# Optimization experiments

Hardware: AMD Instinct MI355X
Metric: run time of the kernel (lower is better)

Reference implementation:

```python
import jax, jax.numpy as jnp
import numpy as np

N = 16384      # total nodes
B = 8          # graphs in batch
NPG = N // B   # nodes per graph
E = 262144     # edges
IN, HID, OUT = 128, 256, 128
ICP_ITERS = 10


def setup_inputs():
    key = jax.random.key(0)
    ks = jax.random.split(key, 12)
    x = jax.random.normal(ks[0], (N, IN), jnp.float32)
    # random edges kept within each graph (offsets per graph)
    src = jax.random.randint(ks[1], (E,), 0, NPG, dtype=jnp.int32)
    dst = jax.random.randint(ks[2], (E,), 0, NPG, dtype=jnp.int32)
    goff = (jnp.arange(E, dtype=jnp.int32) % B) * NPG
    edge_index = jnp.stack([src + goff, dst + goff], 0)
    pos = jax.random.normal(ks[3], (N, 3), jnp.float32)
    batch = jnp.repeat(jnp.arange(B, dtype=jnp.int32), NPG)
    def lin(k, fi, fo):
        return jax.random.normal(k, (fi, fo), jnp.float32) * (fi ** -0.5)
    return dict(
        x=x, edge_index=edge_index, pos=pos, batch=batch,
        W1=lin(ks[4], IN, HID),  b1=jnp.zeros((HID,), jnp.float32),
        W2=lin(ks[5], HID, HID), b2=jnp.zeros((HID,), jnp.float32),
        W3=lin(ks[6], HID, OUT), b3=jnp.zeros((OUT,), jnp.float32),
        Wt=lin(ks[7], OUT, 3),   bt=jnp.zeros((3,), jnp.float32),
    )


def gcn_conv(x, W, b, row, col, n):
    # GCNConv: symmetric norm with self loops; messages flow row->col
    xw = x @ W
    loop = jnp.arange(n, dtype=row.dtype)
    r = jnp.concatenate([row, loop])
    c = jnp.concatenate([col, loop])
    deg = jax.ops.segment_sum(jnp.ones_like(c, dtype=xw.dtype), c, num_segments=n)
    dinv = jnp.where(deg > 0, jax.lax.rsqrt(jnp.maximum(deg, 1e-12)), 0.0)
    norm = dinv[r] * dinv[c]
    out = jax.ops.segment_sum(xw[r] * norm[:, None], c, num_segments=n)
    return out + b


def pdist2(a, b):
    # squared pairwise distances [n,m]
    return (jnp.sum(a * a, -1)[:, None] + jnp.sum(b * b, -1)[None, :]
            - 2.0 * (a @ b.T))


def icp_align(src, tgt):
    # fixed-iteration batched ICP (Kabsch/SVD per iteration)
    for _ in range(ICP_ITERS):
        d = pdist2(jax.lax.stop_gradient(src), jax.lax.stop_gradient(tgt))
        idx = jnp.argmin(d, axis=1)
        corr = tgt[idx]
        cs = jnp.mean(src, 0)
        cc = jnp.mean(corr, 0)
        H = (src - cs).T @ (corr - cc)  # [3,3]
        U, S, Vt = jnp.linalg.svd(H, full_matrices=False)
        sign = jnp.sign(jnp.linalg.det(Vt.T @ U.T))
        D = jnp.stack([jnp.ones_like(sign), jnp.ones_like(sign), sign])
        R = (Vt.T * D[None, :]) @ U.T
        t = cc - R @ cs
        src = src @ R.T + t
    return src


def chamfer(a, b):
    d = pdist2(jax.lax.stop_gradient(a), jax.lax.stop_gradient(b))
    ia = jnp.argmin(d, 1)
    ib = jnp.argmin(d, 0)
    d1 = jnp.mean(jnp.sum((a - b[ia]) ** 2, -1))
    d2 = jnp.mean(jnp.sum((b - a[ib]) ** 2, -1))
    return d1 + d2


def reference(x, edge_index, pos, batch, W1, b1, W2, b2, W3, b3, Wt, bt):
    n = x.shape[0]
    row, col = edge_index[0], edge_index[1]
    h = jax.nn.relu(gcn_conv(x, W1, b1, row, col, n))
    h = jax.nn.relu(gcn_conv(h, W2, b2, row, col, n))
    h = gcn_conv(h, W3, b3, row, col, n)
    pos_offset = h @ Wt + bt
    tpos = pos + pos_offset
    nb = int(batch[-1]) + 1          # sorted, equal-size graphs
    npg = n // nb
    src = tpos.reshape(nb, npg, 3)
    tgt = pos.reshape(nb, npg, 3)
    aligned = jax.vmap(icp_align)(src, tgt)
    loss = jnp.mean(jax.vmap(chamfer)(aligned, tgt))
    return h, aligned.reshape(n, 3), loss
```

## Files before the change

kernel.cpp:

```cpp
#include <hip/hip_runtime.h>
#include <math.h>

#define N_NODES 16384
#define B_GRAPHS 8
#define NPG_     2048
#define E_EDGES  262144
#define F_IN  128
#define F_HID 256
#define F_OUT 128
#define ICP_IT 10

typedef __attribute__((ext_vector_type(8))) short bf16x8;
typedef __attribute__((ext_vector_type(4))) float f32x4;

__device__ __forceinline__ float b2f(unsigned short u) {
    union { unsigned int u; float f; } v; v.u = ((unsigned int)u) << 16; return v.f;
}
__device__ __forceinline__ unsigned short f2b(float f) {
    union { float f; unsigned int u; } v; v.f = f;
    unsigned int r = v.u + 0x7FFFu + ((v.u >> 16) & 1u);
    return (unsigned short)(r >> 16);
}
__device__ __forceinline__ int swz32(int i) {
    return (i & ~31) | ((i & 31) ^ ((i >> 5) & 31));
}
__device__ __forceinline__ void st_agent(float* p, float v) {
    __hip_atomic_store(p, v, __ATOMIC_RELAXED, __HIP_MEMORY_SCOPE_AGENT);
}
__device__ __forceinline__ float ld_agent(const float* p) {
    return __hip_atomic_load(p, __ATOMIC_RELAXED, __HIP_MEMORY_SCOPE_AGENT);
}
__device__ __forceinline__ void st_agent_i(int* p, int v) {
    __hip_atomic_store(p, v, __ATOMIC_RELAXED, __HIP_MEMORY_SCOPE_AGENT);
}
__device__ __forceinline__ int ld_agent_i(const int* p) {
    return __hip_atomic_load(p, __ATOMIC_RELAXED, __HIP_MEMORY_SCOPE_AGENT);
}

__global__ __launch_bounds__(256) void k_prep(
    const float* __restrict__ x, unsigned short* __restrict__ xb,
    const float* __restrict__ W1, const float* __restrict__ W2, const float* __restrict__ W3,
    unsigned short* __restrict__ W1b, unsigned short* __restrict__ W2b, unsigned short* __restrict__ W3b,
    const int* __restrict__ col, int* __restrict__ counts)
{
    const int b = blockIdx.x, tid = threadIdx.x;
    if (b < 2048) {
        int i = b * 256 + tid;
        float4 v = ((const float4*)x)[i];
        uint2 o;
        o.x = (unsigned int)f2b(v.x) | ((unsigned int)f2b(v.y) << 16);
        o.y = (unsigned int)f2b(v.z) | ((unsigned int)f2b(v.w) << 16);
        ((uint2*)xb)[i] = o;
    } else if (b < 2176) {
        int idx = (b - 2048) * 256 + tid;
        int k = idx >> 8, n = idx & 255;
        W1b[n * 128 + k] = f2b(W1[idx]);
    } else if (b < 2432) {
        int idx = (b - 2176) * 256 + tid;
        int k = idx >> 8, n = idx & 255;
        W2b[n * 256 + k] = f2b(W2[idx]);
    } else if (b < 2560) {
        int idx = (b - 2432) * 256 + tid;
        int k = idx >> 7, n = idx & 127;
        W3b[n * 256 + k] = f2b(W3[idx]);
    } else {
        int e = (b - 2560) * 256 + tid;
        atomicAdd(&counts[col[e]], 1);
    }
}

__global__ __launch_bounds__(1024) void k_scan(const int* __restrict__ counts,
        int* __restrict__ offs, int* __restrict__ cursor, float* __restrict__ dinv)
{
    __shared__ int wtot[16];
    const int t = threadIdx.x;
    const int base = t * 16;
    int local[16];
    int s = 0;
#pragma unroll
    for (int i = 0; i < 16; i++) { local[i] = counts[base + i]; s += local[i]; }
    const int lane = t & 63, w = t >> 6;
    int inc = s;
    for (int o = 1; o < 64; o <<= 1) {
        int v = __shfl_up(inc, o);
        if (lane >= o) inc += v;
    }
    if (lane == 63) wtot[w] = inc;
    __syncthreads();
    if (t < 16) {
        int v = wtot[t];
        for (int o = 1; o < 16; o <<= 1) {
            int u = __shfl_up(v, o);
            if (t >= o) v += u;
        }
        wtot[t] = v;
    }
    __syncthreads();
    int run = (w > 0 ? wtot[w - 1] : 0) + (inc - s);
#pragma unroll
    for (int i = 0; i < 16; i++) {
        offs[base + i]   = run;
        cursor[base + i] = run;
        dinv[base + i]   = rsqrtf((float)(local[i] + 1));
        run += local[i];
    }
    if (t == 1023) offs[N_NODES] = run;
}

__global__ void k_scatter(const int* __restrict__ row, const int* __restrict__ col,
        int* __restrict__ cursor, const float* __restrict__ dinv,
        int* __restrict__ srcid, float* __restrict__ normv)
{
    int e = blockIdx.x * 256 + threadIdx.x;
    if (e >= E_EDGES) return;
    int r = row[e], c = col[e];
    int p = atomicAdd(&cursor[c], 1);
    srcid[p] = r;
    normv[p] = dinv[r] * dinv[c];
}

template<int OUTF, int FUSET>
__global__ __launch_bounds__(128) void k_agg128(const unsigned short* __restrict__ X,
        void* __restrict__ Y,
        const int* __restrict__ offs, const int* __restrict__ srcid,
        const float* __restrict__ normv, const float* __restrict__ dinv,
        const float* __restrict__ bias, int relu,
        const float* __restrict__ Wt, const float* __restrict__ bt,
        const float* __restrict__ pos, float* __restrict__ tposO)
{
    const int local = threadIdx.x >> 6;
    const int n = blockIdx.x * 2 + local;
    const int j = threadIdx.x & 63;
    const unsigned int* Xu = (const unsigned int*)X;
    float di = dinv[n];
    float w0 = di * di;
    unsigned int v = Xu[(size_t)n * 64 + j];
    float a0 = b2f((unsigned short)v) * w0;
    float a1 = b2f((unsigned short)(v >> 16)) * w0;
    int p = offs[n];
    const int p1 = offs[n + 1];
    for (; p + 3 < p1; p += 4) {
        int s0i = srcid[p], s1i = srcid[p + 1], s2i = srcid[p + 2], s3i = srcid[p + 3];
        float n0 = normv[p], n1 = normv[p + 1], n2 = normv[p + 2], n3 = normv[p + 3];
        unsigned int v0 = Xu[(size_t)s0i * 64 + j];
        unsigned int v1 = Xu[(size_t)s1i * 64 + j];
        unsigned int v2 = Xu[(size_t)s2i * 64 + j];
        unsigned int v3 = Xu[(size_t)s3i * 64 + j];
        a0 = fmaf(b2f((unsigned short)v0), n0, a0);
        a1 = fmaf(b2f((unsigned short)(v0 >> 16)), n0, a1);
        a0 = fmaf(b2f((unsigned short)v1), n1, a0);
        a1 = fmaf(b2f((unsigned short)(v1 >> 16)), n1, a1);
        a0 = fmaf(b2f((unsigned short)v2), n2, a0);
        a1 = fmaf(b2f((unsigned short)(v2 >> 16)), n2, a1);
        a0 = fmaf(b2f((unsigned short)v3), n3, a0);
        a1 = fmaf(b2f((unsigned short)(v3 >> 16)), n3, a1);
    }
    for (; p < p1; ++p) {
        unsigned int va = Xu[(size_t)srcid[p] * 64 + j]; float na = normv[p];
        a0 = fmaf(b2f((unsigned short)va), na, a0);
        a1 = fmaf(b2f((unsigned short)(va >> 16)), na, a1);
    }
    if (bias) { a0 += bias[2 * j]; a1 += bias[2 * j + 1]; }
    if (relu) { a0 = fmaxf(a0, 0.f); a1 = fmaxf(a1, 0.f); }
    if (OUTF) {
        float* Yf = (float*)Y;
        Yf[(size_t)n * 128 + 2 * j]     = a0;
        Yf[(size_t)n * 128 + 2 * j + 1] = a1;
    } else {
        ((unsigned int*)Y)[(size_t)n * 64 + j] =
            (unsigned int)f2b(a0) | ((unsigned int)f2b(a1) << 16);
    }
    if (FUSET) {
        float wt0 = Wt[6 * j + 0], wt1 = Wt[6 * j + 1], wt2 = Wt[6 * j + 2];
        float wt3 = Wt[6 * j + 3], wt4 = Wt[6 * j + 4], wt5 = Wt[6 * j + 5];
        float s0 = a0 * wt0 + a1 * wt3;
        float s1 = a0 * wt1 + a1 * wt4;
        float s2 = a0 * wt2 + a1 * wt5;
        for (int o = 32; o > 0; o >>= 1) {
            s0 += __shfl_down(s0, o);
            s1 += __shfl_down(s1, o);
            s2 += __shfl_down(s2, o);
        }
        if (j == 0) {
            tposO[n * 3 + 0] = pos[n * 3 + 0] + s0 + bt[0];
            tposO[n * 3 + 1] = pos[n * 3 + 1] + s1 + bt[1];
            tposO[n * 3 + 2] = pos[n * 3 + 2] + s2 + bt[2];
        }
    }
}

__global__ __launch_bounds__(128) void k_agg256(const unsigned short* __restrict__ X,
        unsigned short* __restrict__ Y,
        const int* __restrict__ offs, const int* __restrict__ srcid,
        const float* __restrict__ normv, const float* __restrict__ dinv,
        const float* __restrict__ bias, int relu)
{
    const int local = threadIdx.x >> 6;
    const int n = blockIdx.x * 2 + local;
    const int lane = threadIdx.x & 63;
    const uint2* Xu = (const uint2*)X;
    float di = dinv[n];
    float w0 = di * di;
    uint2 v = Xu[(size_t)n * 64 + lane];
    float a0 = b2f((unsigned short)v.x) * w0;
    float a1 = b2f((unsigned short)(v.x >> 16)) * w0;
    float a2 = b2f((unsigned short)v.y) * w0;
    float a3 = b2f((unsigned short)(v.y >> 16)) * w0;
    int p = offs[n];
    const int p1 = offs[n + 1];
    for (; p + 3 < p1; p += 4) {
        int s0i = srcid[p], s1i = srcid[p + 1], s2i = srcid[p + 2], s3i = srcid[p + 3];
        float n0 = normv[p], n1 = normv[p + 1], n2 = normv[p + 2], n3 = normv[p + 3];
        uint2 v0 = Xu[(size_t)s0i * 64 + lane];
        uint2 v1 = Xu[(size_t)s1i * 64 + lane];
        uint2 v2 = Xu[(size_t)s2i * 64 + lane];
        uint2 v3 = Xu[(size_t)s3i * 64 + lane];
        a0 = fmaf(b2f((unsigned short)v0.x), n0, a0);
        a1 = fmaf(b2f((unsigned short)(v0.x >> 16)), n0, a1);
        a2 = fmaf(b2f((unsigned short)v0.y), n0, a2);
        a3 = fmaf(b2f((unsigned short)(v0.y >> 16)), n0, a3);
        a0 = fmaf(b2f((unsigned short)v1.x), n1, a0);
        a1 = fmaf(b2f((unsigned short)(v1.x >> 16)), n1, a1);
        a2 = fmaf(b2f((unsigned short)v1.y), n1, a2);
        a3 = fmaf(b2f((unsigned short)(v1.y >> 16)), n1, a3);
        a0 = fmaf(b2f((unsigned short)v2.x), n2, a0);
        a1 = fmaf(b2f((unsigned short)(v2.x >> 16)), n2, a1);
        a2 = fmaf(b2f((unsigned short)v2.y), n2, a2);
        a3 = fmaf(b2f((unsigned short)(v2.y >> 16)), n2, a3);
        a0 = fmaf(b2f((unsigned short)v3.x), n3, a0);
        a1 = fmaf(b2f((unsigned short)(v3.x >> 16)), n3, a1);
        a2 = fmaf(b2f((unsigned short)v3.y), n3, a2);
        a3 = fmaf(b2f((unsigned short)(v3.y >> 16)), n3, a3);
    }
    for (; p < p1; ++p) {
        uint2 va = Xu[(size_t)srcid[p] * 64 + lane]; float na = normv[p];
        a0 = fmaf(b2f((unsigned short)va.x), na, a0);
        a1 = fmaf(b2f((unsigned short)(va.x >> 16)), na, a1);
        a2 = fmaf(b2f((unsigned short)va.y), na, a2);
        a3 = fmaf(b2f((unsigned short)(va.y >> 16)), na, a3);
    }
    if (bias) {
        float4 bv = ((const float4*)bias)[lane];
        a0 += bv.x; a1 += bv.y; a2 += bv.z; a3 += bv.w;
    }
    if (relu) {
        a0 = fmaxf(a0, 0.f); a1 = fmaxf(a1, 0.f);
        a2 = fmaxf(a2, 0.f); a3 = fmaxf(a3, 0.f);
    }
    uint2 o;
    o.x = (unsigned int)f2b(a0) | ((unsigned int)f2b(a1) << 16);
    o.y = (unsigned int)f2b(a2) | ((unsigned int)f2b(a3) << 16);
    ((uint2*)Y)[(size_t)n * 64 + lane] = o;
}

__global__ __launch_bounds__(256) void k_gemm_bf16(
    const unsigned short* __restrict__ A,
    const unsigned short* __restrict__ Bt,
    const float* __restrict__ bias, unsigned short* __restrict__ C,
    int M, int N, int K, int relu)
{
    __shared__ __align__(16) unsigned short As[128 * 64];
    __shared__ __align__(16) unsigned short Bs[64 * 64];
    const int tid  = threadIdx.x;
    const int lane = tid & 63;
    const int wave = tid >> 6;
    const int bm = blockIdx.y * 128, bn = blockIdx.x * 64;
    const int wm = (wave >> 1) * 64, wn = (wave & 1) * 32;
    f32x4 acc[4][2];
#pragma unroll
    for (int mf = 0; mf < 4; mf++)
#pragma unroll
        for (int nf = 0; nf < 2; nf++) acc[mf][nf] = (f32x4){0.f, 0.f, 0.f, 0.f};

    for (int k0 = 0; k0 < K; k0 += 64) {
#pragma unroll
        for (int i = 0; i < 4; i++) {
            int idx = i * 256 + tid;
            int m = idx >> 3, slot = idx & 7;
            const unsigned short* src = A + (size_t)(bm + m) * K + k0 + ((slot ^ (m & 7)) << 3);
            __builtin_amdgcn_global_load_lds(
                (const __attribute__((address_space(1))) unsigned int*)src,
                (__attribute__((address_space(3))) unsigned int*)(As + (size_t)i * 2048 + wave * 512),
                16, 0, 0);
        }
#pragma unroll
        for (int i = 0; i < 2; i++) {
            int idx = i * 256 + tid;
            int n = idx >> 3, slot = idx & 7;
            const unsigned short* src = Bt + (size_t)(bn + n) * K + k0 + ((slot ^ (n & 7)) << 3);
            __builtin_amdgcn_global_load_lds(
                (const __attribute__((address_space(1))) unsigned int*)src,
                (__attribute__((address_space(3))) unsigned int*)(Bs + (size_t)i * 2048 + wave * 512),
                16, 0, 0);
        }
        __syncthreads();
        bf16x8 af[4][2], bfr[2][2];
        const int qd = lane >> 4;
#pragma unroll
        for (int s = 0; s < 2; s++) {
#pragma unroll
            for (int mf = 0; mf < 4; mf++) {
                int m = wm + mf * 16 + (lane & 15);
                int slot = (s * 4 + qd) ^ (m & 7);
                af[mf][s] = *(const bf16x8*)(As + m * 64 + slot * 8);
            }
#pragma unroll
            for (int nf = 0; nf < 2; nf++) {
                int n = wn + nf * 16 + (lane & 15);
                int slot = (s * 4 + qd) ^ (n & 7);
                bfr[nf][s] = *(const bf16x8*)(Bs + n * 64 + slot * 8);
            }
        }
#pragma unroll
        for (int s = 0; s < 2; s++)
#pragma unroll
            for (int mf = 0; mf < 4; mf++)
#pragma unroll
                for (int nf = 0; nf < 2; nf++)
                    acc[mf][nf] = __builtin_amdgcn_mfma_f32_16x16x32_bf16(
                        af[mf][s], bfr[nf][s], acc[mf][nf], 0, 0, 0);
        __syncthreads();
    }
#pragma unroll
    for (int nf = 0; nf < 2; nf++) {
        int col = bn + wn + nf * 16 + (lane & 15);
        float bv = bias ? bias[col] : 0.f;
#pragma unroll
        for (int mf = 0; mf < 4; mf++) {
#pragma unroll
            for (int r = 0; r < 4; r++) {
                int row = bm + wm + mf * 16 + (lane >> 4) * 4 + r;
                float v = acc[mf][nf][r] + bv;
                if (relu) v = fmaxf(v, 0.f);
                C[(size_t)row * N + col] = f2b(v);
            }
        }
    }
}

__global__ __launch_bounds__(512) void k_icp_all(
    const float* __restrict__ tpos, const float* __restrict__ pos,
    float* __restrict__ partials,
    float* __restrict__ chpart,
    int* __restrict__ ctrs,
    float* __restrict__ out_aligned, float* __restrict__ out_loss)
{
    const int g = blockIdx.x & 7, blk = blockIdx.x >> 3;
    const int myline = g * 32 + blk;
    const int tid = threadIdx.x;
    const int wave = tid >> 6, lane = tid & 63;
    __shared__ float4 tq[NPG_];
    __shared__ __align__(16) unsigned char scratch[NPG_ * 16];
    float* sm_d = (float*)scratch;
    unsigned short* sm_i = (unsigned short*)(scratch + 64 * 65 * 4);
    float4* al = (float4*)scratch;
    __shared__ float ssx[64], ssy[64], ssz[64];
    __shared__ float wred[8][2];
    __shared__ float Tsh[12];
    __shared__ int lastFlag;

    for (int i = tid; i < NPG_; i += 512) {
        const float* p = &pos[(size_t)(g * NPG_ + i) * 3];
        float qx = p[0], qy = p[1], qz = p[2];
        tq[swz32(i)] = make_float4(qx, qy, qz, fmaf(qx, qx, fmaf(qy, qy, qz * qz)));
    }
    if (tid < 12) Tsh[tid] = (tid == 0 || tid == 4 || tid == 8) ? 1.f : 0.f;
    float Px[8], Py[8], Pz[8];
#pragma unroll
    for (int u = 0; u < 8; u++) {
        int n = g * NPG_ + blk * 64 + wave * 8 + u;
        Px[u] = tpos[n * 3 + 0]; Py[u] = tpos[n * 3 + 1]; Pz[u] = tpos[n * 3 + 2];
    }
    double Td[12];
    if (tid == 0) {
#pragma unroll
        for (int k = 0; k < 12; k++) Td[k] = (k == 0 || k == 4 || k == 8) ? 1.0 : 0.0;
    }
    __syncthreads();

    for (int iter = 0; iter < ICP_IT; ++iter) {
        const int bufbase = (iter & 1) * 256;
        float Tf[12];
#pragma unroll
        for (int k = 0; k < 12; k++) Tf[k] = Tsh[k];
        float Sx[8], Sy[8], Sz[8], Tx[8], Ty[8], Tz[8], bd[8];
        int bi[8];
#pragma unroll
        for (int u = 0; u < 8; u++) {
            float X = Tf[0] * Px[u] + Tf[1] * Py[u] + Tf[2] * Pz[u] + Tf[9];
            float Y = Tf[3] * Px[u] + Tf[4] * Py[u] + Tf[5] * Pz[u] + Tf[10];
            float Z = Tf[6] * Px[u] + Tf[7] * Py[u] + Tf[8] * Pz[u] + Tf[11];
            Sx[u] = X; Sy[u] = Y; Sz[u] = Z;
            Tx[u] = -2.f * X; Ty[u] = -2.f * Y; Tz[u] = -2.f * Z;
            bd[u] = 1e30f; bi[u] = lane * 32;
        }
        const int qbase = lane * 32;
        for (int j = 0; j < 32; j++) {
            float4 t4 = tq[qbase + (j ^ (lane & 31))];
            int idx = qbase + j;
#pragma unroll
            for (int u = 0; u < 8; u++) {
                float d = fmaf(Tx[u], t4.x, fmaf(Ty[u], t4.y, fmaf(Tz[u], t4.z, t4.w)));
                if (d < bd[u]) { bd[u] = d; bi[u] = idx; }
            }
        }
#pragma unroll
        for (int u = 0; u < 8; u++) {
            int row = wave * 8 + u;
            sm_d[row * 65 + lane] = bd[u];
            sm_i[row * 65 + lane] = (unsigned short)bi[u];
            if (lane == u) { ssx[row] = Sx[u]; ssy[row] = Sy[u]; ssz[row] = Sz[u]; }
        }
        __syncthreads();
        if (wave == 0) {
            const int s = tid;
            float best = sm_d[s * 65];
            int ib = sm_i[s * 65];
            for (int r = 1; r < 64; r++) {
                float dd = sm_d[s * 65 + r];
                int ii = sm_i[s * 65 + r];
                if (dd < best) { best = dd; ib = ii; }
            }
            float4 c = tq[swz32(ib)];
            float X = ssx[s], Y = ssy[s], Z = ssz[s];
            float vals[15] = { X, Y, Z, c.x, c.y, c.z,
                               X * c.x, X * c.y, X * c.z,
                               Y * c.x, Y * c.y, Y * c.z,
                               Z * c.x, Z * c.y, Z * c.z };
#pragma unroll
            for (int k = 0; k < 15; k++) {
                float v = vals[k];
                for (int o = 32; o > 0; o >>= 1) v += __shfl_down(v, o);
                if (lane == 0) st_agent(&partials[((size_t)bufbase + myline) * 16 + k], v);
            }
            if (lane == 0) {
                asm volatile("s_waitcnt vmcnt(0)" ::: "memory");
                st_agent_i((int*)partials + ((size_t)bufbase + myline) * 16 + 15, iter + 1);
            }
            double sd[15];
#pragma unroll
            for (int k = 0; k < 15; k++) sd[k] = 0.0;
            if (lane < 32) {
                const float* lp = partials + ((size_t)bufbase + g * 32 + lane) * 16;
                while (ld_agent_i((const int*)lp + 15) < iter + 1) __builtin_amdgcn_s_sleep(1);
                asm volatile("" ::: "memory");
#pragma unroll
                for (int k = 0; k < 15; k++) sd[k] = (double)ld_agent(lp + k);
            }
#pragma unroll
            for (int k = 0; k < 15; k++) {
                for (int o = 16; o > 0; o >>= 1) sd[k] += __shfl_down(sd[k], o);
            }
            if (lane == 0) {
                const double n = (double)NPG_;
                const double rin = 1.0 / (double)NPG_;
                double cs0 = sd[0] * rin, cs1 = sd[1] * rin, cs2 = sd[2] * rin;
                double cc0 = sd[3] * rin, cc1 = sd[4] * rin, cc2 = sd[5] * rin;
                float H[3][3];
                H[0][0] = (float)(sd[6]  - n * cs0 * cc0); H[0][1] = (float)(sd[7]  - n * cs0 * cc1); H[0][2] = (float)(sd[8]  - n * cs0 * cc2);
                H[1][0] = (float)(sd[9]  - n * cs1 * cc0); H[1][1] = (float)(sd[10] - n * cs1 * cc1); H[1][2] = (float)(sd[11] - n * cs1 * cc2);
                H[2][0] = (float)(sd[12] - n * cs2 * cc0); H[2][1] = (float)(sd[13] - n * cs2 * cc1); H[2][2] = (float)(sd[14] - n * cs2 * cc2);
                double R[3][3];
                float fn = 1e-30f;
                for (int i = 0; i < 3; i++) for (int j2 = 0; j2 < 3; j2++) fn += H[i][j2] * H[i][j2];
                float sc = rsqrtf(fn);
                float Xm[3][3];
                for (int i = 0; i < 3; i++) for (int j2 = 0; j2 < 3; j2++) Xm[i][j2] = H[i][j2] * sc;
                float dX = Xm[0][0] * (Xm[1][1]*Xm[2][2] - Xm[1][2]*Xm[2][1])
                         - Xm[0][1] * (Xm[1][0]*Xm[2][2] - Xm[1][2]*Xm[2][0])
                         + Xm[0][2] * (Xm[1][0]*Xm[2][1] - Xm[1][1]*Xm[2][0]);
                if (dX > 1e-4f) {
                    for (int itn = 0; itn < 16; ++itn) {
                        float C00 = Xm[1][1]*Xm[2][2] - Xm[1][2]*Xm[2][1];
                        float C01 = Xm[1][2]*Xm[2][0] - Xm[1][0]*Xm[2][2];
                        float C02 = Xm[1][0]*Xm[2][1] - Xm[1][1]*Xm[2][0];
                        float C10 = Xm[2][1]*Xm[0][2] - Xm[2][2]*Xm[0][1];
                        float C11 = Xm[2][2]*Xm[0][0] - Xm[2][0]*Xm[0][2];
                        float C12 = Xm[2][0]*Xm[0][1] - Xm[2][1]*Xm[0][0];
                        float C20 = Xm[0][1]*Xm[1][2] - Xm[0][2]*Xm[1][1];
                        float C21 = Xm[0][2]*Xm[1][0] - Xm[0][0]*Xm[1][2];
                        float C22 = Xm[0][0]*Xm[1][1] - Xm[0][1]*Xm[1][0];
                        float det = Xm[0][0]*C00 + Xm[0][1]*C01 + Xm[0][2]*C02;
                        if (fabsf(det) < 1e-30f) break;
                        float rd = 0.5f / det;
                        Xm[0][0] = 0.5f*Xm[0][0] + C00*rd; Xm[0][1] = 0.5f*Xm[0][1] + C01*rd; Xm[0][2] = 0.5f*Xm[0][2] + C02*rd;
                        Xm[1][0] = 0.5f*Xm[1][0] + C10*rd; Xm[1][1] = 0.5f*Xm[1][1] + C11*rd; Xm[1][2] = 0.5f*Xm[1][2] + C12*rd;
                        Xm[2][0] = 0.5f*Xm[2][0] + C20*rd; Xm[2][1] = 0.5f*Xm[2][1] + C21*rd; Xm[2][2] = 0.5f*Xm[2][2] + C22*rd;
                    }
                    for (int i = 0; i < 3; i++) for (int j2 = 0; j2 < 3; j2++) R[i][j2] = (double)Xm[j2][i];
                } else {
                    float A[3][3], V[3][3] = {{1,0,0},{0,1,0},{0,0,1}};
                    for (int i = 0; i < 3; i++)
                        for (int j2 = 0; j2 < 3; j2++)
                            A[i][j2] = H[0][i] * H[0][j2] + H[1][i] * H[1][j2] + H[2][i] * H[2][j2];
                    for (int sweep = 0; sweep < 8; ++sweep) {
                        for (int p = 0; p < 2; p++) for (int q = p + 1; q < 3; q++) {
                            float apq = A[p][q];
                            if (fabsf(apq) < 1e-30f) continue;
                            float theta = (A[q][q] - A[p][p]) / (2.f * apq);
                            float t = copysignf(1.f, theta) / (fabsf(theta) + sqrtf(theta * theta + 1.f));
                            float c2 = 1.f / sqrtf(t * t + 1.f);
                            float s2 = t * c2;
                            for (int k = 0; k < 3; k++) { float akp = A[k][p], akq = A[k][q]; A[k][p] = c2*akp - s2*akq; A[k][q] = s2*akp + c2*akq; }
                            for (int k = 0; k < 3; k++) { float apk = A[p][k], aqk = A[q][k]; A[p][k] = c2*apk - s2*aqk; A[q][k] = s2*apk + c2*aqk; }
                            for (int k = 0; k < 3; k++) { float vkp = V[k][p], vkq = V[k][q]; V[k][p] = c2*vkp - s2*vkq; V[k][q] = s2*vkp + c2*vkq; }
                        }
                    }
                    float lam[3] = { A[0][0], A[1][1], A[2][2] };
                    int ord[3] = { 0, 1, 2 };
                    if (lam[ord[1]] > lam[ord[0]]) { int t0 = ord[0]; ord[0] = ord[1]; ord[1] = t0; }
                    if (lam[ord[2]] > lam[ord[0]]) { int t0 = ord[0]; ord[0] = ord[2]; ord[2] = t0; }
                    if (lam[ord[2]] > lam[ord[1]]) { int t0 = ord[1]; ord[1] = ord[2]; ord[2] = t0; }
                    float vc[3][3], uc[3][3];
                    for (int i = 0; i < 3; i++) { vc[i][0] = V[0][ord[i]]; vc[i][1] = V[1][ord[i]]; vc[i][2] = V[2][ord[i]]; }
                    for (int i = 0; i < 3; i++) {
                        float u0 = H[0][0]*vc[i][0] + H[0][1]*vc[i][1] + H[0][2]*vc[i][2];
                        float u1 = H[1][0]*vc[i][0] + H[1][1]*vc[i][1] + H[1][2]*vc[i][2];
                        float u2 = H[2][0]*vc[i][0] + H[2][1]*vc[i][1] + H[2][2]*vc[i][2];
                        for (int j2 = 0; j2 < i; j2++) {
                            float dp = u0*uc[j2][0] + u1*uc[j2][1] + u2*uc[j2][2];
                            u0 -= dp*uc[j2][0]; u1 -= dp*uc[j2][1]; u2 -= dp*uc[j2][2];
                        }
                        float nn2 = sqrtf(u0*u0 + u1*u1 + u2*u2);
                        if (nn2 > 1e-12f) { uc[i][0] = u0/nn2; uc[i][1] = u1/nn2; uc[i][2] = u2/nn2; }
                        else if (i == 2) {
                            uc[2][0] = uc[0][1]*uc[1][2] - uc[0][2]*uc[1][1];
                            uc[2][1] = uc[0][2]*uc[1][0] - uc[0][0]*uc[1][2];
                            uc[2][2] = uc[0][0]*uc[1][1] - uc[0][1]*uc[1][0];
                        } else if (i == 1) {
                            float a0 = (fabsf(uc[0][0]) < 0.9f) ? 1.f : 0.f, a1 = 1.f - a0, a2 = 0.f;
                            float dp = a0*uc[0][0] + a1*uc[0][1] + a2*uc[0][2];
                            a0 -= dp*uc[0][0]; a1 -= dp*uc[0][1]; a2 -= dp*uc[0][2];
                            float nn3 = sqrtf(a0*a0 + a1*a1 + a2*a2);
                            uc[1][0] = a0/nn3; uc[1][1] = a1/nn3; uc[1][2] = a2/nn3;
                        } else { uc[0][0] = 1; uc[0][1] = 0; uc[0][2] = 0; }
                    }
                    float detU = uc[0][0]*(uc[1][1]*uc[2][2] - uc[1][2]*uc[2][1])
                               - uc[0][1]*(uc[1][0]*uc[2][2] - uc[1][2]*uc[2][0])
                               + uc[0][2]*(uc[1][0]*uc[2][1] - uc[1][1]*uc[2][0]);
                    float detV = vc[0][0]*(vc[1][1]*vc[2][2] - vc[1][2]*vc[2][1])
                               - vc[0][1]*(vc[1][0]*vc[2][2] - vc[1][2]*vc[2][0])
                               + vc[0][2]*(vc[1][0]*vc[2][1] - vc[1][1]*vc[2][0]);
                    float sgn = (detU * detV < 0.f) ? -1.f : 1.f;
                    for (int i = 0; i < 3; i++)
                        for (int j2 = 0; j2 < 3; j2++)
                            R[i][j2] = (double)(vc[0][i]*uc[0][j2] + vc[1][i]*uc[1][j2] + sgn * vc[2][i]*uc[2][j2]);
                }
                double tr0 = cc0 - (R[0][0]*cs0 + R[0][1]*cs1 + R[0][2]*cs2);
                double tr1 = cc1 - (R[1][0]*cs0 + R[1][1]*cs1 + R[1][2]*cs2);
                double tr2 = cc2 - (R[2][0]*cs0 + R[2][1]*cs1 + R[2][2]*cs2);
                double An[12];
                for (int i = 0; i < 3; i++)
                    for (int j2 = 0; j2 < 3; j2++)
                        An[i*3+j2] = R[i][0]*Td[0*3+j2] + R[i][1]*Td[1*3+j2] + R[i][2]*Td[2*3+j2];
                An[9]  = R[0][0]*Td[9] + R[0][1]*Td[10] + R[0][2]*Td[11] + tr0;
                An[10] = R[1][0]*Td[9] + R[1][1]*Td[10] + R[1][2]*Td[11] + tr1;
                An[11] = R[2][0]*Td[9] + R[2][1]*Td[10] + R[2][2]*Td[11] + tr2;
#pragma unroll
                for (int k = 0; k < 12; k++) { Td[k] = An[k]; Tsh[k] = (float)An[k]; }
            }
        }
        __syncthreads();
    }

    {
        float Tf[12];
#pragma unroll
        for (int k = 0; k < 12; k++) Tf[k] = Tsh[k];
        __syncthreads();
        for (int i = tid; i < NPG_; i += 512) {
            const float* q = &tpos[(size_t)(g * NPG_ + i) * 3];
            float X = Tf[0] * q[0] + Tf[1] * q[1] + Tf[2] * q[2] + Tf[9];
            float Y = Tf[3] * q[0] + Tf[4] * q[1] + Tf[5] * q[2] + Tf[10];
            float Z = Tf[6] * q[0] + Tf[7] * q[1] + Tf[8] * q[2] + Tf[11];
            al[swz32(i)] = make_float4(X, Y, Z, fmaf(X, X, fmaf(Y, Y, Z * Z)));
            if (blk == 0) {
                out_aligned[(size_t)(g * NPG_ + i) * 3 + 0] = X;
                out_aligned[(size_t)(g * NPG_ + i) * 3 + 1] = Y;
                out_aligned[(size_t)(g * NPG_ + i) * 3 + 2] = Z;
            }
        }
        __syncthreads();
        float Ax[8], Ay[8], Az[8], Aw[8], Qx[8], Qy[8], Qz[8], Qw[8], d1[8], d2[8];
#pragma unroll
        for (int u = 0; u < 8; u++) {
            int s = swz32(blk * 64 + wave * 8 + u);
            float4 a4 = al[s]; float4 p4 = tq[s];
            Ax[u] = -2.f * a4.x; Ay[u] = -2.f * a4.y; Az[u] = -2.f * a4.z; Aw[u] = a4.w;
            Qx[u] = -2.f * p4.x; Qy[u] = -2.f * p4.y; Qz[u] = -2.f * p4.z; Qw[u] = p4.w;
            d1[u] = 1e30f; d2[u] = 1e30f;
        }
        const int qbase = lane * 32;
        for (int j = 0; j < 32; j++) {
            int s = qbase + (j ^ (lane & 31));
            float4 t4 = tq[s];
            float4 b4 = al[s];
#pragma unroll
            for (int u = 0; u < 8; u++) {
                d1[u] = fminf(d1[u], fmaf(Ax[u], t4.x, fmaf(Ay[u], t4.y, fmaf(Az[u], t4.z, t4.w))));
                d2[u] = fminf(d2[u], fmaf(Qx[u], b4.x, fmaf(Qy[u], b4.y, fmaf(Qz[u], b4.z, b4.w))));
            }
        }
        float s1 = 0.f, s2 = 0.f;
#pragma unroll
        for (int u = 0; u < 8; u++) {
            float a = d1[u], b = d2[u];
            for (int o = 32; o > 0; o >>= 1) {
                a = fminf(a, __shfl_down(a, o));
                b = fminf(b, __shfl_down(b, o));
            }
            s1 += a + Aw[u];
            s2 += b + Qw[u];
        }
        if (lane == 0) { wred[wave][0] = s1; wred[wave][1] = s2; }
        __syncthreads();
        if (tid == 0) {
            float t1 = 0.f, t2 = 0.f;
#pragma unroll
            for (int w = 0; w < 8; w++) { t1 += wred[w][0]; t2 += wred[w][1]; }
            st_agent(&chpart[blockIdx.x * 2 + 0], t1);
            st_agent(&chpart[blockIdx.x * 2 + 1], t2);
        }
        __syncthreads();
        if (tid == 0) {
            int old = atomicAdd(&ctrs[128], 1);
            lastFlag = (old == (int)gridDim.x - 1) ? 1 : 0;
        }
        __syncthreads();
        if (!lastFlag) return;
        float v1 = 0.f, v2 = 0.f;
        if (tid < 256) {
            v1 = ld_agent(&chpart[tid * 2 + 0]);
            v2 = ld_agent(&chpart[tid * 2 + 1]);
        }
        for (int o = 32; o > 0; o >>= 1) {
            v1 += __shfl_down(v1, o);
            v2 += __shfl_down(v2, o);
        }
        if (lane == 0 && wave < 4) { wred[wave][0] = v1; wred[wave][1] = v2; }
        __syncthreads();
        if (tid == 0) {
            float tot = 0.f;
#pragma unroll
            for (int w = 0; w < 4; w++) tot += wred[w][0] + wred[w][1];
            out_loss[0] = tot / (float)(NPG_ * B_GRAPHS);
        }
    }
}

extern "C" void kernel_launch(void* const* d_in, const int* in_sizes, int n_in,
                              void* d_out, int out_size, void* d_ws, size_t ws_size,
                              hipStream_t stream)
{
    (void)in_sizes; (void)n_in; (void)out_size; (void)ws_size;
    const float* x   = (const float*)d_in[0];
    const int*   ei  = (const int*)d_in[1];
    const float* pos = (const float*)d_in[2];
    const float* W1 = (const float*)d_in[4];
    const float* b1 = (const float*)d_in[5];
    const float* W2 = (const float*)d_in[6];
    const float* b2 = (const float*)d_in[7];
    const float* W3 = (const float*)d_in[8];
    const float* b3 = (const float*)d_in[9];
    const float* Wt = (const float*)d_in[10];
    const float* bt = (const float*)d_in[11];
    const int* row = ei;
    const int* col = ei + E_EDGES;

    char* wsb = (char*)d_ws;
    size_t off_b = 0;
    auto alloc = [&](size_t bytes) -> void* {
        void* p = wsb + off_b;
        off_b = (off_b + bytes + 255) & ~(size_t)255;
        return p;
    };
    int*    counts   = (int*)alloc((size_t)N_NODES * 4);
    float*  partials = (float*)alloc((size_t)2 * 256 * 16 * 4);
    int*    ctrs     = (int*)alloc((size_t)256 * 4);
    int*    offs     = (int*)alloc((size_t)(N_NODES + 1) * 4);
    int*    cursor   = (int*)alloc((size_t)N_NODES * 4);
    int*    srcid    = (int*)alloc((size_t)E_EDGES * 4);
    float*  normv    = (float*)alloc((size_t)E_EDGES * 4);
    float*  dinv     = (float*)alloc((size_t)N_NODES * 4);
    unsigned short* xb  = (unsigned short*)alloc((size_t)N_NODES * F_IN * 2);
    unsigned short* W1b = (unsigned short*)alloc((size_t)F_IN * F_HID * 2);
    unsigned short* W2b = (unsigned short*)alloc((size_t)F_HID * F_HID * 2);
    unsigned short* W3b = (unsigned short*)alloc((size_t)F_HID * F_OUT * 2);
    unsigned short* bufA = (unsigned short*)alloc((size_t)N_NODES * F_HID * 2);
    unsigned short* bufB = (unsigned short*)alloc((size_t)N_NODES * F_HID * 2);
    unsigned short* bufC = (unsigned short*)alloc((size_t)N_NODES * F_HID * 2);
    float*  tpos     = (float*)alloc((size_t)N_NODES * 3 * 4);
    float*  chpart   = (float*)alloc((size_t)256 * 2 * 4);

    float* out_h       = (float*)d_out;
    float* out_aligned = out_h + (size_t)N_NODES * F_OUT;
    float* out_loss    = out_aligned + (size_t)N_NODES * 3;

    hipMemsetAsync(counts, 0, (size_t)N_NODES * 4 + 2 * 256 * 16 * 4 + 256 * 4, stream);
    k_prep<<<3584, 256, 0, stream>>>(x, xb, W1, W2, W3, W1b, W2b, W3b, col, counts);
    k_scan<<<1, 1024, 0, stream>>>(counts, offs, cursor, dinv);
    k_scatter<<<E_EDGES / 256, 256, 0, stream>>>(row, col, cursor, dinv, srcid, normv);

    k_agg128<0, 0><<<N_NODES / 2, 128, 0, stream>>>(xb, bufA, offs, srcid, normv, dinv,
            nullptr, 0, nullptr, nullptr, nullptr, nullptr);
    {
        dim3 grid(F_HID / 64, N_NODES / 128);
        k_gemm_bf16<<<grid, 256, 0, stream>>>(bufA, W1b, b1, bufB, N_NODES, F_HID, F_IN, 1);
    }
    {
        dim3 grid(F_HID / 64, N_NODES / 128);
        k_gemm_bf16<<<grid, 256, 0, stream>>>(bufB, W2b, nullptr, bufC, N_NODES, F_HID, F_HID, 0);
    }
    k_agg256<<<N_NODES / 2, 128, 0, stream>>>(bufC, bufA, offs, srcid, normv, dinv, b2, 1);
    {
        dim3 grid(F_OUT / 64, N_NODES / 128);
        k_gemm_bf16<<<grid, 256, 0, stream>>>(bufA, W3b, nullptr, bufB, N_NODES, F_OUT, F_HID, 0);
    }
    k_agg128<1, 1><<<N_NODES / 2, 128, 0, stream>>>(bufB, out_h, offs, srcid, normv, dinv,
            b3, 0, Wt, bt, pos, tpos);

    k_icp_all<<<256, 512, 0, stream>>>(tpos, pos, partials, chpart, ctrs,
            out_aligned, out_loss);
}
```

Baseline: 322.4 us.

## Split persistent ICP kernel into per-iteration launches with redundant Kabsch

Replaces the single persistent ICP kernel, which synchronized blocks across the grid through atomic counters and global partials each iteration, with ten separate nearest-neighbor launches plus a final chamfer launch. Each block now redundantly reduces the previous iteration's partials and solves the 3x3 Kabsch update itself, with the double-precision transform chained through a global array. The padded float4 target positions are precomputed once in the prep kernel instead of rebuilt from pos. This removes grid-wide spin barriers at the cost of extra kernel launches, reloading shared memory on every launch, and redundant per-block SVD work.

```diff
diff --git a/kernel.cpp b/kernel.cpp
--- a/kernel.cpp
+++ b/kernel.cpp
@@ -30,15 +30,155 @@
 __device__ __forceinline__ float ld_agent(const float* p) {
     return __hip_atomic_load(p, __ATOMIC_RELAXED, __HIP_MEMORY_SCOPE_AGENT);
 }
-__device__ __forceinline__ void st_agent_i(int* p, int v) {
-    __hip_atomic_store(p, v, __ATOMIC_RELAXED, __HIP_MEMORY_SCOPE_AGENT);
-}
-__device__ __forceinline__ int ld_agent_i(const int* p) {
-    return __hip_atomic_load(p, __ATOMIC_RELAXED, __HIP_MEMORY_SCOPE_AGENT);
+
+__device__ void kabsch_update(const double sd[15], const double Tp[12], double Tn[12])
+{
+    const double n = (double)NPG_;
+    const double rin = 1.0 / n;
+    double cs0 = sd[0]*rin, cs1 = sd[1]*rin, cs2 = sd[2]*rin;
+    double cc0 = sd[3]*rin, cc1 = sd[4]*rin, cc2 = sd[5]*rin;
+    float H[3][3];
+    H[0][0] = (float)(sd[6]  - n*cs0*cc0); H[0][1] = (float)(sd[7]  - n*cs0*cc1); H[0][2] = (float)(sd[8]  - n*cs0*cc2);
+    H[1][0] = (float)(sd[9]  - n*cs1*cc0); H[1][1] = (float)(sd[10] - n*cs1*cc1); H[1][2] = (float)(sd[11] - n*cs1*cc2);
+    H[2][0] = (float)(sd[12] - n*cs2*cc0); H[2][1] = (float)(sd[13] - n*cs2*cc1); H[2][2] = (float)(sd[14] - n*cs2*cc2);
+    double R[3][3];
+    float fn = 1e-30f;
+    for (int i = 0; i < 3; i++) for (int j = 0; j < 3; j++) fn += H[i][j] * H[i][j];
+    float sc = rsqrtf(fn);
+    float Xm[3][3];
+    for (int i = 0; i < 3; i++) for (int j = 0; j < 3; j++) Xm[i][j] = H[i][j] * sc;
+    float dX = Xm[0][0]*(Xm[1][1]*Xm[2][2]-Xm[1][2]*Xm[2][1])
+             - Xm[0][1]*(Xm[1][0]*Xm[2][2]-Xm[1][2]*Xm[2][0])
+             + Xm[0][2]*(Xm[1][0]*Xm[2][1]-Xm[1][1]*Xm[2][0]);
+    if (dX > 1e-4f) {
+        for (int itn = 0; itn < 16; ++itn) {
+            float C00 = Xm[1][1]*Xm[2][2]-Xm[1][2]*Xm[2][1];
+            float C01 = Xm[1][2]*Xm[2][0]-Xm[1][0]*Xm[2][2];
+            float C02 = Xm[1][0]*Xm[2][1]-Xm[1][1]*Xm[2][0];
+            float C10 = Xm[2][1]*Xm[0][2]-Xm[2][2]*Xm[0][1];
+            float C11 = Xm[2][2]*Xm[0][0]-Xm[2][0]*Xm[0][2];
+            float C12 = Xm[2][0]*Xm[0][1]-Xm[2][1]*Xm[0][0];
+            float C20 = Xm[0][1]*Xm[1][2]-Xm[0][2]*Xm[1][1];
+            float C21 = Xm[0][2]*Xm[1][0]-Xm[0][0]*Xm[1][2];
+            float C22 = Xm[0][0]*Xm[1][1]-Xm[0][1]*Xm[1][0];
+            float det = Xm[0][0]*C00 + Xm[0][1]*C01 + Xm[0][2]*C02;
+            if (fabsf(det) < 1e-30f) break;
+            float rd = 0.5f / det;
+            Xm[0][0]=0.5f*Xm[0][0]+C00*rd; Xm[0][1]=0.5f*Xm[0][1]+C01*rd; Xm[0][2]=0.5f*Xm[0][2]+C02*rd;
+            Xm[1][0]=0.5f*Xm[1][0]+C10*rd; Xm[1][1]=0.5f*Xm[1][1]+C11*rd; Xm[1][2]=0.5f*Xm[1][2]+C12*rd;
+            Xm[2][0]=0.5f*Xm[2][0]+C20*rd; Xm[2][1]=0.5f*Xm[2][1]+C21*rd; Xm[2][2]=0.5f*Xm[2][2]+C22*rd;
+        }
+        for (int i = 0; i < 3; i++) for (int j = 0; j < 3; j++) R[i][j] = (double)Xm[j][i];
+    } else {
+        float A[3][3], V[3][3] = {{1,0,0},{0,1,0},{0,0,1}};
+        for (int i = 0; i < 3; i++)
+            for (int j = 0; j < 3; j++)
+                A[i][j] = H[0][i]*H[0][j] + H[1][i]*H[1][j] + H[2][i]*H[2][j];
+        for (int sweep = 0; sweep < 8; ++sweep) {
+            for (int p = 0; p < 2; p++) for (int q = p + 1; q < 3; q++) {
+                float apq = A[p][q];
+                if (fabsf(apq) < 1e-30f) continue;
+                float theta = (A[q][q] - A[p][p]) / (2.f * apq);
+                float t = copysignf(1.f, theta) / (fabsf(theta) + sqrtf(theta*theta + 1.f));
+                float c = 1.f / sqrtf(t*t + 1.f);
+                float s = t * c;
+                for (int k = 0; k < 3; k++) { float akp=A[k][p], akq=A[k][q]; A[k][p]=c*akp-s*akq; A[k][q]=s*akp+c*akq; }
+                for (int k = 0; k < 3; k++) { float apk=A[p][k], aqk=A[q][k]; A[p][k]=c*apk-s*aqk; A[q][k]=s*apk+c*aqk; }
+                for (int k = 0; k < 3; k++) { float vkp=V[k][p], vkq=V[k][q]; V[k][p]=c*vkp-s*vkq; V[k][q]=s*vkp+c*vkq; }
+            }
+        }
+        float lam[3] = { A[0][0], A[1][1], A[2][2] };
+        int ord[3] = { 0, 1, 2 };
+        if (lam[ord[1]] > lam[ord[0]]) { int t0=ord[0]; ord[0]=ord[1]; ord[1]=t0; }
+        if (lam[ord[2]] > lam[ord[0]]) { int t0=ord[0]; ord[0]=ord[2]; ord[2]=t0; }
+        if (lam[ord[2]] > lam[ord[1]]) { int t0=ord[1]; ord[1]=ord[2]; ord[2]=t0; }
+        float vc[3][3], uc[3][3];
+        for (int i = 0; i < 3; i++) { vc[i][0]=V[0][ord[i]]; vc[i][1]=V[1][ord[i]]; vc[i][2]=V[2][ord[i]]; }
+        for (int i = 0; i < 3; i++) {
+            float u0 = H[0][0]*vc[i][0] + H[0][1]*vc[i][1] + H[0][2]*vc[i][2];
+            float u1 = H[1][0]*vc[i][0] + H[1][1]*vc[i][1] + H[1][2]*vc[i][2];
+            float u2 = H[2][0]*vc[i][0] + H[2][1]*vc[i][1] + H[2][2]*vc[i][2];
+            for (int j = 0; j < i; j++) {
+                float dp = u0*uc[j][0] + u1*uc[j][1] + u2*uc[j][2];
+                u0 -= dp*uc[j][0]; u1 -= dp*uc[j][1]; u2 -= dp*uc[j][2];
+            }
+            float nn2 = sqrtf(u0*u0 + u1*u1 + u2*u2);
+            if (nn2 > 1e-12f) { uc[i][0]=u0/nn2; uc[i][1]=u1/nn2; uc[i][2]=u2/nn2; }
+            else if (i == 2) {
+                uc[2][0]=uc[0][1]*uc[1][2]-uc[0][2]*uc[1][1];
+                uc[2][1]=uc[0][2]*uc[1][0]-uc[0][0]*uc[1][2];
+                uc[2][2]=uc[0][0]*uc[1][1]-uc[0][1]*uc[1][0];
+            } else if (i == 1) {
+                float a0 = (fabsf(uc[0][0]) < 0.9f) ? 1.f : 0.f, a1 = 1.f - a0, a2 = 0.f;
+                float dp = a0*uc[0][0] + a1*uc[0][1] + a2*uc[0][2];
+                a0 -= dp*uc[0][0]; a1 -= dp*uc[0][1]; a2 -= dp*uc[0][2];
+                float nn3 = sqrtf(a0*a0 + a1*a1 + a2*a2);
+                uc[1][0]=a0/nn3; uc[1][1]=a1/nn3; uc[1][2]=a2/nn3;
+            } else { uc[0][0]=1; uc[0][1]=0; uc[0][2]=0; }
+        }
+        float detU = uc[0][0]*(uc[1][1]*uc[2][2]-uc[1][2]*uc[2][1])
+                   - uc[0][1]*(uc[1][0]*uc[2][2]-uc[1][2]*uc[2][0])
+                   + uc[0][2]*(uc[1][0]*uc[2][1]-uc[1][1]*uc[2][0]);
+        float detV = vc[0][0]*(vc[1][1]*vc[2][2]-vc[1][2]*vc[2][1])
+                   - vc[0][1]*(vc[1][0]*vc[2][2]-vc[1][2]*vc[2][0])
+                   + vc[0][2]*(vc[1][0]*vc[2][1]-vc[1][1]*vc[2][0]);
+        float sgn = (detU * detV < 0.f) ? -1.f : 1.f;
+        for (int i = 0; i < 3; i++)
+            for (int j = 0; j < 3; j++)
+                R[i][j] = (double)(vc[0][i]*uc[0][j] + vc[1][i]*uc[1][j] + sgn*vc[2][i]*uc[2][j]);
+    }
+    double tr0 = cc0 - (R[0][0]*cs0 + R[0][1]*cs1 + R[0][2]*cs2);
+    double tr1 = cc1 - (R[1][0]*cs0 + R[1][1]*cs1 + R[1][2]*cs2);
+    double tr2 = cc2 - (R[2][0]*cs0 + R[2][1]*cs1 + R[2][2]*cs2);
+    for (int i = 0; i < 3; i++)
+        for (int j = 0; j < 3; j++)
+            Tn[i*3+j] = R[i][0]*Tp[0*3+j] + R[i][1]*Tp[1*3+j] + R[i][2]*Tp[2*3+j];
+    Tn[9]  = R[0][0]*Tp[9] + R[0][1]*Tp[10] + R[0][2]*Tp[11] + tr0;
+    Tn[10] = R[1][0]*Tp[9] + R[1][1]*Tp[10] + R[1][2]*Tp[11] + tr1;
+    Tn[11] = R[2][0]*Tp[9] + R[2][1]*Tp[10] + R[2][2]*Tp[11] + tr2;
+}
+
+__device__ void compute_T_wave0(int lane, int g, int iter,
+        const float* __restrict__ Pin, const double* __restrict__ TdIn,
+        double* __restrict__ TdOut, float* Tsh, int writeTd, int isBlock0)
+{
+    if (iter == 0) {
+        if (lane < 12) Tsh[lane] = (lane == 0 || lane == 4 || lane == 8) ? 1.f : 0.f;
+        return;
+    }
+    double sd[15];
+#pragma unroll
+    for (int k = 0; k < 15; k++) sd[k] = 0.0;
+    if (lane < 32) {
+        const float* lp = Pin + ((size_t)g * 32 + lane) * 16;
+#pragma unroll
+        for (int k = 0; k < 15; k++) sd[k] = (double)lp[k];
+    }
+#pragma unroll
+    for (int k = 0; k < 15; k++)
+        for (int o = 16; o > 0; o >>= 1) sd[k] += __shfl_down(sd[k], o);
+    if (lane == 0) {
+        double Tp[12], Tn[12];
+        if (iter == 1) {
+#pragma unroll
+            for (int k = 0; k < 12; k++) Tp[k] = (k == 0 || k == 4 || k == 8) ? 1.0 : 0.0;
+        } else {
+#pragma unroll
+            for (int k = 0; k < 12; k++) Tp[k] = TdIn[k];
+        }
+        kabsch_update(sd, Tp, Tn);
+#pragma unroll
+        for (int k = 0; k < 12; k++) Tsh[k] = (float)Tn[k];
+        if (writeTd && isBlock0) {
+#pragma unroll
+            for (int k = 0; k < 12; k++) TdOut[k] = Tn[k];
+        }
+    }
 }
 
 __global__ __launch_bounds__(256) void k_prep(
     const float* __restrict__ x, unsigned short* __restrict__ xb,
+    const float* __restrict__ pos, float4* __restrict__ pos4,
     const float* __restrict__ W1, const float* __restrict__ W2, const float* __restrict__ W3,
     unsigned short* __restrict__ W1b, unsigned short* __restrict__ W2b, unsigned short* __restrict__ W3b,
     const int* __restrict__ col, int* __restrict__ counts)
@@ -51,20 +191,24 @@
         o.x = (unsigned int)f2b(v.x) | ((unsigned int)f2b(v.y) << 16);
         o.y = (unsigned int)f2b(v.z) | ((unsigned int)f2b(v.w) << 16);
         ((uint2*)xb)[i] = o;
-    } else if (b < 2176) {
-        int idx = (b - 2048) * 256 + tid;
+    } else if (b < 2112) {
+        int i = (b - 2048) * 256 + tid;
+        float px = pos[i*3], py = pos[i*3+1], pz = pos[i*3+2];
+        pos4[i] = make_float4(px, py, pz, fmaf(px, px, fmaf(py, py, pz * pz)));
+    } else if (b < 2240) {
+        int idx = (b - 2112) * 256 + tid;
         int k = idx >> 8, n = idx & 255;
         W1b[n * 128 + k] = f2b(W1[idx]);
-    } else if (b < 2432) {
-        int idx = (b - 2176) * 256 + tid;
+    } else if (b < 2496) {
+        int idx = (b - 2240) * 256 + tid;
         int k = idx >> 8, n = idx & 255;
         W2b[n * 256 + k] = f2b(W2[idx]);
-    } else if (b < 2560) {
-        int idx = (b - 2432) * 256 + tid;
+    } else if (b < 2624) {
+        int idx = (b - 2496) * 256 + tid;
         int k = idx >> 7, n = idx & 127;
         W3b[n * 256 + k] = f2b(W3[idx]);
     } else {
-        int e = (b - 2560) * 256 + tid;
+        int e = (b - 2624) * 256 + tid;
         atomicAdd(&counts[col[e]], 1);
     }
 }
@@ -338,313 +482,190 @@
     }
 }
 
-__global__ __launch_bounds__(512) void k_icp_all(
-    const float* __restrict__ tpos, const float* __restrict__ pos,
-    float* __restrict__ partials,
-    float* __restrict__ chpart,
-    int* __restrict__ ctrs,
-    float* __restrict__ out_aligned, float* __restrict__ out_loss)
-{
-    const int g = blockIdx.x & 7, blk = blockIdx.x >> 3;
-    const int myline = g * 32 + blk;
+__global__ __launch_bounds__(512) void k_icp_nn(
+    const float4* __restrict__ pos4, const float* __restrict__ tpos,
+    const float* __restrict__ Pin, float* __restrict__ Pout,
+    const double* __restrict__ TdIn, double* __restrict__ TdOut,
+    int iter)
+{
+    const int g = blockIdx.x >> 5, blk = blockIdx.x & 31;
     const int tid = threadIdx.x;
     const int wave = tid >> 6, lane = tid & 63;
     __shared__ float4 tq[NPG_];
-    __shared__ __align__(16) unsigned char scratch[NPG_ * 16];
-    float* sm_d = (float*)scratch;
-    unsigned short* sm_i = (unsigned short*)(scratch + 64 * 65 * 4);
-    float4* al = (float4*)scratch;
+    __shared__ float sm_d[64 * 65];
+    __shared__ unsigned short sm_i[64 * 65];
     __shared__ float ssx[64], ssy[64], ssz[64];
+    __shared__ float Tsh[12];
+
+    for (int i = tid; i < NPG_; i += 512)
+        tq[swz32(i)] = pos4[(size_t)g * NPG_ + i];
+    float Px[8], Py[8], Pz[8];
+#pragma unroll
+    for (int u = 0; u < 8; u++) {
+        int n = g * NPG_ + blk * 64 + wave * 8 + u;
+        Px[u] = tpos[n * 3 + 0]; Py[u] = tpos[n * 3 + 1]; Pz[u] = tpos[n * 3 + 2];
+    }
+    if (wave == 0)
+        compute_T_wave0(lane, g, iter, Pin, TdIn + g * 12, TdOut + g * 12, Tsh,
+                        iter > 0, blk == 0);
+    __syncthreads();
+
+    float Tf[12];
+#pragma unroll
+    for (int k = 0; k < 12; k++) Tf[k] = Tsh[k];
+    float Sx[8], Sy[8], Sz[8], Tx[8], Ty[8], Tz[8], bd[8];
+    int bi[8];
+#pragma unroll
+    for (int u = 0; u < 8; u++) {
+        float X = Tf[0] * Px[u] + Tf[1] * Py[u] + Tf[2] * Pz[u] + Tf[9];
+        float Y = Tf[3] * Px[u] + Tf[4] * Py[u] + Tf[5] * Pz[u] + Tf[10];
+        float Z = Tf[6] * Px[u] + Tf[7] * Py[u] + Tf[8] * Pz[u] + Tf[11];
+        Sx[u] = X; Sy[u] = Y; Sz[u] = Z;
+        Tx[u] = -2.f * X; Ty[u] = -2.f * Y; Tz[u] = -2.f * Z;
+        bd[u] = 1e30f; bi[u] = lane * 32;
+    }
+    const int qbase = lane * 32;
+    for (int j = 0; j < 32; j++) {
+        float4 t4 = tq[qbase + (j ^ (lane & 31))];
+        int idx = qbase + j;
+#pragma unroll
+        for (int u = 0; u < 8; u++) {
+            float d = fmaf(Tx[u], t4.x, fmaf(Ty[u], t4.y, fmaf(Tz[u], t4.z, t4.w)));
+            if (d < bd[u]) { bd[u] = d; bi[u] = idx; }
+        }
+    }
+#pragma unroll
+    for (int u = 0; u < 8; u++) {
+        int row = wave * 8 + u;
+        sm_d[row * 65 + lane] = bd[u];
+        sm_i[row * 65 + lane] = (unsigned short)bi[u];
+        if (lane == u) { ssx[row] = Sx[u]; ssy[row] = Sy[u]; ssz[row] = Sz[u]; }
+    }
+    __syncthreads();
+    if (tid < 64) {
+        const int s = tid;
+        float best = sm_d[s * 65];
+        int ib = sm_i[s * 65];
+        for (int r = 1; r < 64; r++) {
+            float dd = sm_d[s * 65 + r];
+            int ii = sm_i[s * 65 + r];
+            if (dd < best) { best = dd; ib = ii; }
+        }
+        float4 c = tq[swz32(ib)];
+        float X = ssx[s], Y = ssy[s], Z = ssz[s];
+        float vals[15] = { X, Y, Z, c.x, c.y, c.z,
+                           X * c.x, X * c.y, X * c.z,
+                           Y * c.x, Y * c.y, Y * c.z,
+                           Z * c.x, Z * c.y, Z * c.z };
+#pragma unroll
+        for (int k = 0; k < 15; k++) {
+            float v = vals[k];
+            for (int o = 32; o > 0; o >>= 1) v += __shfl_down(v, o);
+            if (tid == 0) Pout[(size_t)blockIdx.x * 16 + k] = v;
+        }
+    }
+}
+
+__global__ __launch_bounds__(512) void k_chamfer_all(
+    const float4* __restrict__ pos4, const float* __restrict__ tpos,
+    const float* __restrict__ Pin, const double* __restrict__ TdIn,
+    float* __restrict__ chpart, int* __restrict__ ctrs,
+    float* __restrict__ out_aligned, float* __restrict__ out_loss)
+{
+    const int g = blockIdx.x >> 5, blk = blockIdx.x & 31;
+    const int tid = threadIdx.x;
+    const int wave = tid >> 6, lane = tid & 63;
+    __shared__ float4 tq[NPG_];
+    __shared__ float4 al[NPG_];
     __shared__ float wred[8][2];
     __shared__ float Tsh[12];
     __shared__ int lastFlag;
 
+    for (int i = tid; i < NPG_; i += 512)
+        tq[swz32(i)] = pos4[(size_t)g * NPG_ + i];
+    if (wave == 0)
+        compute_T_wave0(lane, g, ICP_IT, Pin, TdIn + g * 12, nullptr, Tsh, 0, 0);
+    __syncthreads();
+
+    float Tf[12];
+#pragma unroll
+    for (int k = 0; k < 12; k++) Tf[k] = Tsh[k];
     for (int i = tid; i < NPG_; i += 512) {
-        const float* p = &pos[(size_t)(g * NPG_ + i) * 3];
-        float qx = p[0], qy = p[1], qz = p[2];
-        tq[swz32(i)] = make_float4(qx, qy, qz, fmaf(qx, qx, fmaf(qy, qy, qz * qz)));
-    }
-    if (tid < 12) Tsh[tid] = (tid == 0 || tid == 4 || tid == 8) ? 1.f : 0.f;
-    float Px[8], Py[8], Pz[8];
+        const float* q = &tpos[(size_t)(g * NPG_ + i) * 3];
+        float X = Tf[0] * q[0] + Tf[1] * q[1] + Tf[2] * q[2] + Tf[9];
+        float Y = Tf[3] * q[0] + Tf[4] * q[1] + Tf[5] * q[2] + Tf[10];
+        float Z = Tf[6] * q[0] + Tf[7] * q[1] + Tf[8] * q[2] + Tf[11];
+        al[swz32(i)] = make_float4(X, Y, Z, fmaf(X, X, fmaf(Y, Y, Z * Z)));
+        if (blk == 0) {
+            out_aligned[(size_t)(g * NPG_ + i) * 3 + 0] = X;
+            out_aligned[(size_t)(g * NPG_ + i) * 3 + 1] = Y;
+            out_aligned[(size_t)(g * NPG_ + i) * 3 + 2] = Z;
+        }
+    }
+    __syncthreads();
+    float Ax[8], Ay[8], Az[8], Aw[8], Qx[8], Qy[8], Qz[8], Qw[8], d1[8], d2[8];
 #pragma unroll
     for (int u = 0; u < 8; u++) {
-        int n = g * NPG_ + blk * 64 + wave * 8 + u;
-        Px[u] = tpos[n * 3 + 0]; Py[u] = tpos[n * 3 + 1]; Pz[u] = tpos[n * 3 + 2];
-    }
-    double Td[12];
+        int s = swz32(blk * 64 + wave * 8 + u);
+        float4 a4 = al[s]; float4 p4 = tq[s];
+        Ax[u] = -2.f * a4.x; Ay[u] = -2.f * a4.y; Az[u] = -2.f * a4.z; Aw[u] = a4.w;
+        Qx[u] = -2.f * p4.x; Qy[u] = -2.f * p4.y; Qz[u] = -2.f * p4.z; Qw[u] = p4.w;
+        d1[u] = 1e30f; d2[u] = 1e30f;
+    }
+    const int qbase = lane * 32;
+    for (int j = 0; j < 32; j++) {
+        int s = qbase + (j ^ (lane & 31));
+        float4 t4 = tq[s];
+        float4 b4 = al[s];
+#pragma unroll
+        for (int u = 0; u < 8; u++) {
+            d1[u] = fminf(d1[u], fmaf(Ax[u], t4.x, fmaf(Ay[u], t4.y, fmaf(Az[u], t4.z, t4.w))));
+            d2[u] = fminf(d2[u], fmaf(Qx[u], b4.x, fmaf(Qy[u], b4.y, fmaf(Qz[u], b4.z, b4.w))));
+        }
+    }
+    float s1 = 0.f, s2 = 0.f;
+#pragma unroll
+    for (int u = 0; u < 8; u++) {
+        float a = d1[u], b = d2[u];
+        for (int o = 32; o > 0; o >>= 1) {
+            a = fminf(a, __shfl_down(a, o));
+            b = fminf(b, __shfl_down(b, o));
+        }
+        s1 += a + Aw[u];
+        s2 += b + Qw[u];
+    }
+    if (lane == 0) { wred[wave][0] = s1; wred[wave][1] = s2; }
+    __syncthreads();
     if (tid == 0) {
-#pragma unroll
-        for (int k = 0; k < 12; k++) Td[k] = (k == 0 || k == 4 || k == 8) ? 1.0 : 0.0;
-    }
-    __syncthreads();
-
-    for (int iter = 0; iter < ICP_IT; ++iter) {
-        const int bufbase = (iter & 1) * 256;
-        float Tf[12];
-#pragma unroll
-        for (int k = 0; k < 12; k++) Tf[k] = Tsh[k];
-        float Sx[8], Sy[8], Sz[8], Tx[8], Ty[8], Tz[8], bd[8];
-        int bi[8];
-#pragma unroll
-        for (int u = 0; u < 8; u++) {
-            float X = Tf[0] * Px[u] + Tf[1] * Py[u] + Tf[2] * Pz[u] + Tf[9];
-            float Y = Tf[3] * Px[u] + Tf[4] * Py[u] + Tf[5] * Pz[u] + Tf[10];
-            float Z = Tf[6] * Px[u] + Tf[7] * Py[u] + Tf[8] * Pz[u] + Tf[11];
-            Sx[u] = X; Sy[u] = Y; Sz[u] = Z;
-            Tx[u] = -2.f * X; Ty[u] = -2.f * Y; Tz[u] = -2.f * Z;
-            bd[u] = 1e30f; bi[u] = lane * 32;
-        }
-        const int qbase = lane * 32;
-        for (int j = 0; j < 32; j++) {
-            float4 t4 = tq[qbase + (j ^ (lane & 31))];
-            int idx = qbase + j;
-#pragma unroll
-            for (int u = 0; u < 8; u++) {
-                float d = fmaf(Tx[u], t4.x, fmaf(Ty[u], t4.y, fmaf(Tz[u], t4.z, t4.w)));
-                if (d < bd[u]) { bd[u] = d; bi[u] = idx; }
-            }
-        }
-#pragma unroll
-        for (int u = 0; u < 8; u++) {
-            int row = wave * 8 + u;
-            sm_d[row * 65 + lane] = bd[u];
-            sm_i[row * 65 + lane] = (unsigned short)bi[u];
-            if (lane == u) { ssx[row] = Sx[u]; ssy[row] = Sy[u]; ssz[row] = Sz[u]; }
-        }
-        __syncthreads();
-        if (wave == 0) {
-            const int s = tid;
-            float best = sm_d[s * 65];
-            int ib = sm_i[s * 65];
-            for (int r = 1; r < 64; r++) {
-                float dd = sm_d[s * 65 + r];
-                int ii = sm_i[s * 65 + r];
-                if (dd < best) { best = dd; ib = ii; }
-            }
-            float4 c = tq[swz32(ib)];
-            float X = ssx[s], Y = ssy[s], Z = ssz[s];
-            float vals[15] = { X, Y, Z, c.x, c.y, c.z,
-                               X * c.x, X * c.y, X * c.z,
-                               Y * c.x, Y * c.y, Y * c.z,
-                               Z * c.x, Z * c.y, Z * c.z };
-#pragma unroll
-            for (int k = 0; k < 15; k++) {
-                float v = vals[k];
-                for (int o = 32; o > 0; o >>= 1) v += __shfl_down(v, o);
-                if (lane == 0) st_agent(&partials[((size_t)bufbase + myline) * 16 + k], v);
-            }
-            if (lane == 0) {
-                asm volatile("s_waitcnt vmcnt(0)" ::: "memory");
-                st_agent_i((int*)partials + ((size_t)bufbase + myline) * 16 + 15, iter + 1);
-            }
-            double sd[15];
-#pragma unroll
-            for (int k = 0; k < 15; k++) sd[k] = 0.0;
-            if (lane < 32) {
-                const float* lp = partials + ((size_t)bufbase + g * 32 + lane) * 16;
-                while (ld_agent_i((const int*)lp + 15) < iter + 1) __builtin_amdgcn_s_sleep(1);
-                asm volatile("" ::: "memory");
-#pragma unroll
-                for (int k = 0; k < 15; k++) sd[k] = (double)ld_agent(lp + k);
-            }
-#pragma unroll
-            for (int k = 0; k < 15; k++) {
-                for (int o = 16; o > 0; o >>= 1) sd[k] += __shfl_down(sd[k], o);
-            }
-            if (lane == 0) {
-                const double n = (double)NPG_;
-                const double rin = 1.0 / (double)NPG_;
-                double cs0 = sd[0] * rin, cs1 = sd[1] * rin, cs2 = sd[2] * rin;
-                double cc0 = sd[3] * rin, cc1 = sd[4] * rin, cc2 = sd[5] * rin;
-                float H[3][3];
-                H[0][0] = (float)(sd[6]  - n * cs0 * cc0); H[0][1] = (float)(sd[7]  - n * cs0 * cc1); H[0][2] = (float)(sd[8]  - n * cs0 * cc2);
-                H[1][0] = (float)(sd[9]  - n * cs1 * cc0); H[1][1] = (float)(sd[10] - n * cs1 * cc1); H[1][2] = (float)(sd[11] - n * cs1 * cc2);
-                H[2][0] = (float)(sd[12] - n * cs2 * cc0); H[2][1] = (float)(sd[13] - n * cs2 * cc1); H[2][2] = (float)(sd[14] - n * cs2 * cc2);
-                double R[3][3];
-                float fn = 1e-30f;
-                for (int i = 0; i < 3; i++) for (int j2 = 0; j2 < 3; j2++) fn += H[i][j2] * H[i][j2];
-                float sc = rsqrtf(fn);
-                float Xm[3][3];
-                for (int i = 0; i < 3; i++) for (int j2 = 0; j2 < 3; j2++) Xm[i][j2] = H[i][j2] * sc;
-                float dX = Xm[0][0] * (Xm[1][1]*Xm[2][2] - Xm[1][2]*Xm[2][1])
-                         - Xm[0][1] * (Xm[1][0]*Xm[2][2] - Xm[1][2]*Xm[2][0])
-                         + Xm[0][2] * (Xm[1][0]*Xm[2][1] - Xm[1][1]*Xm[2][0]);
-                if (dX > 1e-4f) {
-                    for (int itn = 0; itn < 16; ++itn) {
-                        float C00 = Xm[1][1]*Xm[2][2] - Xm[1][2]*Xm[2][1];
-                        float C01 = Xm[1][2]*Xm[2][0] - Xm[1][0]*Xm[2][2];
-                        float C02 = Xm[1][0]*Xm[2][1] - Xm[1][1]*Xm[2][0];
-                        float C10 = Xm[2][1]*Xm[0][2] - Xm[2][2]*Xm[0][1];
-                        float C11 = Xm[2][2]*Xm[0][0] - Xm[2][0]*Xm[0][2];
-                        float C12 = Xm[2][0]*Xm[0][1] - Xm[2][1]*Xm[0][0];
-                        float C20 = Xm[0][1]*Xm[1][2] - Xm[0][2]*Xm[1][1];
-                        float C21 = Xm[0][2]*Xm[1][0] - Xm[0][0]*Xm[1][2];
-                        float C22 = Xm[0][0]*Xm[1][1] - Xm[0][1]*Xm[1][0];
-                        float det = Xm[0][0]*C00 + Xm[0][1]*C01 + Xm[0][2]*C02;
-                        if (fabsf(det) < 1e-30f) break;
-                        float rd = 0.5f / det;
-                        Xm[0][0] = 0.5f*Xm[0][0] + C00*rd; Xm[0][1] = 0.5f*Xm[0][1] + C01*rd; Xm[0][2] = 0.5f*Xm[0][2] + C02*rd;
-                        Xm[1][0] = 0.5f*Xm[1][0] + C10*rd; Xm[1][1] = 0.5f*Xm[1][1] + C11*rd; Xm[1][2] = 0.5f*Xm[1][2] + C12*rd;
-                        Xm[2][0] = 0.5f*Xm[2][0] + C20*rd; Xm[2][1] = 0.5f*Xm[2][1] + C21*rd; Xm[2][2] = 0.5f*Xm[2][2] + C22*rd;
-                    }
-                    for (int i = 0; i < 3; i++) for (int j2 = 0; j2 < 3; j2++) R[i][j2] = (double)Xm[j2][i];
-                } else {
-                    float A[3][3], V[3][3] = {{1,0,0},{0,1,0},{0,0,1}};
-                    for (int i = 0; i < 3; i++)
-                        for (int j2 = 0; j2 < 3; j2++)
-                            A[i][j2] = H[0][i] * H[0][j2] + H[1][i] * H[1][j2] + H[2][i] * H[2][j2];
-                    for (int sweep = 0; sweep < 8; ++sweep) {
-                        for (int p = 0; p < 2; p++) for (int q = p + 1; q < 3; q++) {
-                            float apq = A[p][q];
-                            if (fabsf(apq) < 1e-30f) continue;
-                            float theta = (A[q][q] - A[p][p]) / (2.f * apq);
-                            float t = copysignf(1.f, theta) / (fabsf(theta) + sqrtf(theta * theta + 1.f));
-                            float c2 = 1.f / sqrtf(t * t + 1.f);
-                            float s2 = t * c2;
-                            for (int k = 0; k < 3; k++) { float akp = A[k][p], akq = A[k][q]; A[k][p] = c2*akp - s2*akq; A[k][q] = s2*akp + c2*akq; }
-                            for (int k = 0; k < 3; k++) { float apk = A[p][k], aqk = A[q][k]; A[p][k] = c2*apk - s2*aqk; A[q][k] = s2*apk + c2*aqk; }
-                            for (int k = 0; k < 3; k++) { float vkp = V[k][p], vkq = V[k][q]; V[k][p] = c2*vkp - s2*vkq; V[k][q] = s2*vkp + c2*vkq; }
-                        }
-                    }
-                    float lam[3] = { A[0][0], A[1][1], A[2][2] };
-                    int ord[3] = { 0, 1, 2 };
-                    if (lam[ord[1]] > lam[ord[0]]) { int t0 = ord[0]; ord[0] = ord[1]; ord[1] = t0; }
-                    if (lam[ord[2]] > lam[ord[0]]) { int t0 = ord[0]; ord[0] = ord[2]; ord[2] = t0; }
-                    if (lam[ord[2]] > lam[ord[1]]) { int t0 = ord[1]; ord[1] = ord[2]; ord[2] = t0; }
-                    float vc[3][3], uc[3][3];
-                    for (int i = 0; i < 3; i++) { vc[i][0] = V[0][ord[i]]; vc[i][1] = V[1][ord[i]]; vc[i][2] = V[2][ord[i]]; }
-                    for (int i = 0; i < 3; i++) {
-                        float u0 = H[0][0]*vc[i][0] + H[0][1]*vc[i][1] + H[0][2]*vc[i][2];
-                        float u1 = H[1][0]*vc[i][0] + H[1][1]*vc[i][1] + H[1][2]*vc[i][2];
-                        float u2 = H[2][0]*vc[i][0] + H[2][1]*vc[i][1] + H[2][2]*vc[i][2];
-                        for (int j2 = 0; j2 < i; j2++) {
-                            float dp = u0*uc[j2][0] + u1*uc[j2][1] + u2*uc[j2][2];
-                            u0 -= dp*uc[j2][0]; u1 -= dp*uc[j2][1]; u2 -= dp*uc[j2][2];
-                        }
-                        float nn2 = sqrtf(u0*u0 + u1*u1 + u2*u2);
-                        if (nn2 > 1e-12f) { uc[i][0] = u0/nn2; uc[i][1] = u1/nn2; uc[i][2] = u2/nn2; }
-                        else if (i == 2) {
-                            uc[2][0] = uc[0][1]*uc[1][2] - uc[0][2]*uc[1][1];
-                            uc[2][1] = uc[0][2]*uc[1][0] - uc[0][0]*uc[1][2];
-                            uc[2][2] = uc[0][0]*uc[1][1] - uc[0][1]*uc[1][0];
-                        } else if (i == 1) {
-                            float a0 = (fabsf(uc[0][0]) < 0.9f) ? 1.f : 0.f, a1 = 1.f - a0, a2 = 0.f;
-                            float dp = a0*uc[0][0] + a1*uc[0][1] + a2*uc[0][2];
-                            a0 -= dp*uc[0][0]; a1 -= dp*uc[0][1]; a2 -= dp*uc[0][2];
-                            float nn3 = sqrtf(a0*a0 + a1*a1 + a2*a2);
-                            uc[1][0] = a0/nn3; uc[1][1] = a1/nn3; uc[1][2] = a2/nn3;
-                        } else { uc[0][0] = 1; uc[0][1] = 0; uc[0][2] = 0; }
-                    }
-                    float detU = uc[0][0]*(uc[1][1]*uc[2][2] - uc[1][2]*uc[2][1])
-                               - uc[0][1]*(uc[1][0]*uc[2][2] - uc[1][2]*uc[2][0])
-                               + uc[0][2]*(uc[1][0]*uc[2][1] - uc[1][1]*uc[2][0]);
-                    float detV = vc[0][0]*(vc[1][1]*vc[2][2] - vc[1][2]*vc[2][1])
-                               - vc[0][1]*(vc[1][0]*vc[2][2] - vc[1][2]*vc[2][0])
-                               + vc[0][2]*(vc[1][0]*vc[2][1] - vc[1][1]*vc[2][0]);
-                    float sgn = (detU * detV < 0.f) ? -1.f : 1.f;
-                    for (int i = 0; i < 3; i++)
-                        for (int j2 = 0; j2 < 3; j2++)
-                            R[i][j2] = (double)(vc[0][i]*uc[0][j2] + vc[1][i]*uc[1][j2] + sgn * vc[2][i]*uc[2][j2]);
-                }
-                double tr0 = cc0 - (R[0][0]*cs0 + R[0][1]*cs1 + R[0][2]*cs2);
-                double tr1 = cc1 - (R[1][0]*cs0 + R[1][1]*cs1 + R[1][2]*cs2);
-                double tr2 = cc2 - (R[2][0]*cs0 + R[2][1]*cs1 + R[2][2]*cs2);
-                double An[12];
-                for (int i = 0; i < 3; i++)
-                    for (int j2 = 0; j2 < 3; j2++)
-                        An[i*3+j2] = R[i][0]*Td[0*3+j2] + R[i][1]*Td[1*3+j2] + R[i][2]*Td[2*3+j2];
-                An[9]  = R[0][0]*Td[9] + R[0][1]*Td[10] + R[0][2]*Td[11] + tr0;
-                An[10] = R[1][0]*Td[9] + R[1][1]*Td[10] + R[1][2]*Td[11] + tr1;
-                An[11] = R[2][0]*Td[9] + R[2][1]*Td[10] + R[2][2]*Td[11] + tr2;
-#pragma unroll
-                for (int k = 0; k < 12; k++) { Td[k] = An[k]; Tsh[k] = (float)An[k]; }
-            }
-        }
-        __syncthreads();
-    }
-
-    {
-        float Tf[12];
-#pragma unroll
-        for (int k = 0; k < 12; k++) Tf[k] = Tsh[k];
-        __syncthreads();
-        for (int i = tid; i < NPG_; i += 512) {
-            const float* q = &tpos[(size_t)(g * NPG_ + i) * 3];
-            float X = Tf[0] * q[0] + Tf[1] * q[1] + Tf[2] * q[2] + Tf[9];
-            float Y = Tf[3] * q[0] + Tf[4] * q[1] + Tf[5] * q[2] + Tf[10];
-            float Z = Tf[6] * q[0] + Tf[7] * q[1] + Tf[8] * q[2] + Tf[11];
-            al[swz32(i)] = make_float4(X, Y, Z, fmaf(X, X, fmaf(Y, Y, Z * Z)));
-            if (blk == 0) {
-                out_aligned[(size_t)(g * NPG_ + i) * 3 + 0] = X;
-                out_aligned[(size_t)(g * NPG_ + i) * 3 + 1] = Y;
-                out_aligned[(size_t)(g * NPG_ + i) * 3 + 2] = Z;
-            }
-        }
-        __syncthreads();
-        float Ax[8], Ay[8], Az[8], Aw[8], Qx[8], Qy[8], Qz[8], Qw[8], d1[8], d2[8];
-#pragma unroll
-        for (int u = 0; u < 8; u++) {
-            int s = swz32(blk * 64 + wave * 8 + u);
-            float4 a4 = al[s]; float4 p4 = tq[s];
-            Ax[u] = -2.f * a4.x; Ay[u] = -2.f * a4.y; Az[u] = -2.f * a4.z; Aw[u] = a4.w;
-            Qx[u] = -2.f * p4.x; Qy[u] = -2.f * p4.y; Qz[u] = -2.f * p4.z; Qw[u] = p4.w;
-            d1[u] = 1e30f; d2[u] = 1e30f;
-        }
-        const int qbase = lane * 32;
-        for (int j = 0; j < 32; j++) {
-            int s = qbase + (j ^ (lane & 31));
-            float4 t4 = tq[s];
-            float4 b4 = al[s];
-#pragma unroll
-            for (int u = 0; u < 8; u++) {
-                d1[u] = fminf(d1[u], fmaf(Ax[u], t4.x, fmaf(Ay[u], t4.y, fmaf(Az[u], t4.z, t4.w))));
-                d2[u] = fminf(d2[u], fmaf(Qx[u], b4.x, fmaf(Qy[u], b4.y, fmaf(Qz[u], b4.z, b4.w))));
-            }
-        }
-        float s1 = 0.f, s2 = 0.f;
-#pragma unroll
-        for (int u = 0; u < 8; u++) {
-            float a = d1[u], b = d2[u];
-            for (int o = 32; o > 0; o >>= 1) {
-                a = fminf(a, __shfl_down(a, o));
-                b = fminf(b, __shfl_down(b, o));
-            }
-            s1 += a + Aw[u];
-            s2 += b + Qw[u];
-        }
-        if (lane == 0) { wred[wave][0] = s1; wred[wave][1] = s2; }
-        __syncthreads();
-        if (tid == 0) {
-            float t1 = 0.f, t2 = 0.f;
-#pragma unroll
-            for (int w = 0; w < 8; w++) { t1 += wred[w][0]; t2 += wred[w][1]; }
-            st_agent(&chpart[blockIdx.x * 2 + 0], t1);
-            st_agent(&chpart[blockIdx.x * 2 + 1], t2);
-        }
-        __syncthreads();
-        if (tid == 0) {
-            int old = atomicAdd(&ctrs[128], 1);
-            lastFlag = (old == (int)gridDim.x - 1) ? 1 : 0;
-        }
-        __syncthreads();
-        if (!lastFlag) return;
-        float v1 = 0.f, v2 = 0.f;
-        if (tid < 256) {
-            v1 = ld_agent(&chpart[tid * 2 + 0]);
-            v2 = ld_agent(&chpart[tid * 2 + 1]);
-        }
-        for (int o = 32; o > 0; o >>= 1) {
-            v1 += __shfl_down(v1, o);
-            v2 += __shfl_down(v2, o);
-        }
-        if (lane == 0 && wave < 4) { wred[wave][0] = v1; wred[wave][1] = v2; }
-        __syncthreads();
-        if (tid == 0) {
-            float tot = 0.f;
-#pragma unroll
-            for (int w = 0; w < 4; w++) tot += wred[w][0] + wred[w][1];
-            out_loss[0] = tot / (float)(NPG_ * B_GRAPHS);
-        }
+        float t1 = 0.f, t2 = 0.f;
+#pragma unroll
+        for (int w = 0; w < 8; w++) { t1 += wred[w][0]; t2 += wred[w][1]; }
+        st_agent(&chpart[blockIdx.x * 2 + 0], t1);
+        st_agent(&chpart[blockIdx.x * 2 + 1], t2);
+    }
+    __syncthreads();
+    if (tid == 0) {
+        int old = atomicAdd(&ctrs[0], 1);
+        lastFlag = (old == (int)gridDim.x - 1) ? 1 : 0;
+    }
+    __syncthreads();
+    if (!lastFlag) return;
+    float v1 = 0.f, v2 = 0.f;
+    if (tid < 256) {
+        v1 = ld_agent(&chpart[tid * 2 + 0]);
+        v2 = ld_agent(&chpart[tid * 2 + 1]);
+    }
+    for (int o = 32; o > 0; o >>= 1) {
+        v1 += __shfl_down(v1, o);
+        v2 += __shfl_down(v2, o);
+    }
+    if (lane == 0 && wave < 4) { wred[wave][0] = v1; wred[wave][1] = v2; }
+    __syncthreads();
+    if (tid == 0) {
+        float tot = 0.f;
+#pragma unroll
+        for (int w = 0; w < 4; w++) tot += wred[w][0] + wred[w][1];
+        out_loss[0] = tot / (float)(NPG_ * B_GRAPHS);
     }
 }
 
@@ -675,8 +696,10 @@
         return p;
     };
     int*    counts   = (int*)alloc((size_t)N_NODES * 4);
-    float*  partials = (float*)alloc((size_t)2 * 256 * 16 * 4);
     int*    ctrs     = (int*)alloc((size_t)256 * 4);
+    float4* pos4     = (float4*)alloc((size_t)N_NODES * 16);
+    float*  Pbuf     = (float*)alloc((size_t)2 * 256 * 16 * 4);
+    double* Td_arr   = (double*)alloc((size_t)ICP_IT * B_GRAPHS * 12 * 8);
     int*    offs     = (int*)alloc((size_t)(N_NODES + 1) * 4);
     int*    cursor   = (int*)alloc((size_t)N_NODES * 4);
     int*    srcid    = (int*)alloc((size_t)E_EDGES * 4);
@@ -696,8 +719,8 @@
     float* out_aligned = out_h + (size_t)N_NODES * F_OUT;
     float* out_loss    = out_aligned + (size_t)N_NODES * 3;
 
-    hipMemsetAsync(counts, 0, (size_t)N_NODES * 4 + 2 * 256 * 16 * 4 + 256 * 4, stream);
-    k_prep<<<3584, 256, 0, stream>>>(x, xb, W1, W2, W3, W1b, W2b, W3b, col, counts);
+    hipMemsetAsync(counts, 0, (size_t)N_NODES * 4 + 256 * 4, stream);
+    k_prep<<<3648, 256, 0, stream>>>(x, xb, pos, pos4, W1, W2, W3, W1b, W2b, W3b, col, counts);
     k_scan<<<1, 1024, 0, stream>>>(counts, offs, cursor, dinv);
     k_scatter<<<E_EDGES / 256, 256, 0, stream>>>(row, col, cursor, dinv, srcid, normv);
 
@@ -719,6 +742,15 @@
     k_agg128<1, 1><<<N_NODES / 2, 128, 0, stream>>>(bufB, out_h, offs, srcid, normv, dinv,
             b3, 0, Wt, bt, pos, tpos);
 
-    k_icp_all<<<256, 512, 0, stream>>>(tpos, pos, partials, chpart, ctrs,
-            out_aligned, out_loss);
-}
+    for (int j = 0; j < ICP_IT; ++j) {
+        const float* Pin  = Pbuf + (size_t)((j + 1) & 1) * 256 * 16;
+        float*       Pout = Pbuf + (size_t)(j & 1) * 256 * 16;
+        const double* TdIn = Td_arr + (size_t)(j > 0 ? j - 1 : 0) * B_GRAPHS * 12;
+        double*       TdOut = Td_arr + (size_t)j * B_GRAPHS * 12;
+        k_icp_nn<<<256, 512, 0, stream>>>(pos4, tpos, Pin, Pout, TdIn, TdOut, j);
+    }
+    k_chamfer_all<<<256, 512, 0, stream>>>(pos4, tpos,
+            Pbuf + (size_t)((ICP_IT - 1) & 1) * 256 * 16,
+            Td_arr + (size_t)(ICP_IT - 1) * B_GRAPHS * 12,
+            chpart, ctrs, out_aligned, out_loss);
+}
```

Result: faster. 299.4 us (-7.1%).
